# Kernel optimization log

Hardware: AMD Instinct MI355X
Metric: run time of the kernel (lower is better)

The kernel has to match this reference:

```python
import jax, jax.numpy as jnp
import numpy as np

N_HEAD = 16
ROPE_BASE = 10000.0


def _rope(x):
    # x: (B, T, H, D), interleaved even/odd (GPT-NeoX style)
    B, T, H, D = x.shape
    inv_freq = 1.0 / (ROPE_BASE ** (jnp.arange(0, D, 2, dtype=jnp.float32) / D))
    t = jnp.arange(T, dtype=jnp.float32)
    freqs = t[:, None] * inv_freq[None, :]            # (T, D//2)
    cos = jnp.cos(freqs)[None, :, None, :]            # (1, T, 1, D//2)
    sin = jnp.sin(freqs)[None, :, None, :]
    x1, x2 = x[..., ::2], x[..., 1::2]
    y1 = x1 * cos - x2 * sin
    y2 = x1 * sin + x2 * cos
    return jnp.stack((y1, y2), axis=-1).reshape(B, T, H, D)


def setup_inputs() -> dict:
    key = jax.random.key(0)
    k1, k2, k3 = jax.random.split(key, 3)
    B, T, C = 4, 2048, 1024
    x = jax.random.normal(k1, (B, T, C), dtype=jnp.float32)
    W_attn = jax.random.normal(k2, (C, 3 * C), dtype=jnp.float32) * (1.0 / np.sqrt(C))
    W_proj = jax.random.normal(k3, (C, C), dtype=jnp.float32) * (1.0 / np.sqrt(C))
    return {"x": x, "W_attn": W_attn, "W_proj": W_proj}


def reference(x, W_attn, W_proj):
    B, T, C = x.shape
    H = N_HEAD
    D = C // H
    qkv = jnp.einsum('btc,cf->btf', x, W_attn)        # (B, T, 3C)
    q, k, v = jnp.split(qkv, 3, axis=-1)
    q = _rope(q.reshape(B, T, H, D))
    k = _rope(k.reshape(B, T, H, D))
    v = v.reshape(B, T, H, D)
    # (B, H, T, D)
    q = q.transpose(0, 2, 1, 3)
    k = k.transpose(0, 2, 1, 3)
    v = v.transpose(0, 2, 1, 3)
    scale = 1.0 / np.sqrt(D).astype(np.float32)
    scores = jnp.einsum('bhqd,bhkd->bhqk', q, k) * scale
    causal = jnp.tril(jnp.ones((T, T), dtype=bool))
    scores = jnp.where(causal[None, None], scores, jnp.finfo(scores.dtype).min)
    att = jax.nn.softmax(scores, axis=-1)
    y = jnp.einsum('bhqk,bhkd->bhqd', att, v)         # (B, H, T, D)
    y = y.transpose(0, 2, 1, 3).reshape(B, T, C)
    return jnp.einsum('btc,cf->btf', y, W_proj)
```

## Files before the change

### kernel.cpp

```cpp
#include <hip/hip_runtime.h>
#include <hip/hip_bf16.h>
#include <math.h>

typedef __attribute__((ext_vector_type(8))) __bf16 bf16x8;
typedef __attribute__((ext_vector_type(4))) float f32x4;
typedef __attribute__((ext_vector_type(16))) float f32x16;
typedef __attribute__((ext_vector_type(4))) unsigned short us4;

#define DEVINL static __device__ __forceinline__

DEVINL unsigned short f2bf(float f) {
  union { float f; unsigned int u; } v; v.f = f;
  return (unsigned short)((v.u + 0x7FFFu + ((v.u >> 16) & 1u)) >> 16);
}

DEVINL unsigned short f2bf_hw(float f) {
  __bf16 h = (__bf16)f;
  union { __bf16 h; unsigned short u; } v; v.h = h;
  return v.u;
}

DEVINL unsigned pk2(float a, float b) {
  return (unsigned)f2bf_hw(a) | ((unsigned)f2bf_hw(b) << 16);
}

DEVINL f32x4 mfma16(bf16x8 a, bf16x8 b, f32x4 c) {
  return __builtin_amdgcn_mfma_f32_16x16x32_bf16(a, b, c, 0, 0, 0);
}
DEVINL f32x16 mfma32(bf16x8 a, bf16x8 b, f32x16 c) {
  return __builtin_amdgcn_mfma_f32_32x32x16_bf16(a, b, c, 0, 0, 0);
}

#define GLOAD16(GP, LP)                                                        \
  __builtin_amdgcn_global_load_lds(                                            \
      (const __attribute__((address_space(1))) void*)(GP),                     \
      (__attribute__((address_space(3))) void*)(LP), 16, 0, 0)

static constexpr int kB = 4, kT = 2048, kC = 1024, kH = 16, kD = 64;
static constexpr int kM = kB * kT;

__global__ void cvt_x_kernel(const float* __restrict__ x,
                             unsigned short* __restrict__ xb, int n4) {
  int stride = gridDim.x * blockDim.x;
  for (int i = blockIdx.x * blockDim.x + threadIdx.x; i < n4; i += stride) {
    float4 v = ((const float4*)x)[i];
    us4 o;
    o[0] = f2bf(v.x); o[1] = f2bf(v.y); o[2] = f2bf(v.z); o[3] = f2bf(v.w);
    ((us4*)xb)[i] = o;
  }
}

__global__ void transpose_w_kernel(const float* __restrict__ W,
                                   unsigned short* __restrict__ WT,
                                   int K, int N) {
  __shared__ float tile[32][33];
  int n0 = blockIdx.x * 32, k0 = blockIdx.y * 32;
  int tx = threadIdx.x, ty = threadIdx.y;
#pragma unroll
  for (int i = 0; i < 4; ++i)
    tile[ty + i * 8][tx] = W[(size_t)(k0 + ty + i * 8) * N + n0 + tx];
  __syncthreads();
#pragma unroll
  for (int i = 0; i < 4; ++i)
    WT[(size_t)(n0 + ty + i * 8) * K + k0 + tx] = f2bf(tile[tx][ty + i * 8]);
}

__global__ void rope_table_kernel(float* __restrict__ cosT,
                                  float* __restrict__ sinT) {
  int idx = blockIdx.x * blockDim.x + threadIdx.x;
  if (idx >= kT * 32) return;
  int d2 = idx >> 11, t = idx & 2047;
  double ang = (double)t * pow(10000.0, -(double)d2 / 32.0);
  cosT[idx] = (float)cos(ang);
  sinT[idx] = (float)sin(ang);
}

template <int EPI>
__global__ __launch_bounds__(256) void gemm_bt_kernel(
    const unsigned short* __restrict__ A, const unsigned short* __restrict__ Bt,
    float* __restrict__ Cout, int Ndim, int Kdim,
    const float* __restrict__ cosT, const float* __restrict__ sinT,
    unsigned short* __restrict__ Qr, unsigned short* __restrict__ Kr,
    unsigned short* __restrict__ Vtg) {
  __shared__ unsigned short As[3][128 * 32];
  __shared__ unsigned short Bs[3][128 * 32];
  const int tid = threadIdx.x;
  const int wave = tid >> 6, lane = tid & 63;

  const int nwg = gridDim.x * gridDim.y;
  const int lin = blockIdx.y * gridDim.x + blockIdx.x;
  const int wg = (lin & 7) * (nwg >> 3) + (lin >> 3);
  const int n0 = (wg % gridDim.x) * 128, m0 = (wg / gridDim.x) * 128;

  const int wr = wave >> 1, wc = wave & 1;

  f32x4 acc[4][4] = {};

  const int srow = lane >> 2;
  const int kcol = (lane & 3) * 8;
  const int fr = lane & 15, kk8 = (lane >> 4) * 8;

  auto stage = [&](int k0, int bb) {
#pragma unroll
    for (int o = 0; o < 2; ++o) {
      int s = o * 4 + wave;
      int row = s * 16 + srow;
      GLOAD16(A + (size_t)(m0 + row) * Kdim + k0 + kcol, &As[bb][s * 512]);
      GLOAD16(Bt + (size_t)(n0 + row) * Kdim + k0 + kcol, &Bs[bb][s * 512]);
    }
  };

  const int NT = Kdim >> 5;
  stage(0, 0);
  stage(32, 1);

  for (int t = 0; t < NT; ++t) {
    const int buf = t % 3;
    if (t + 1 < NT) {
      asm volatile("s_waitcnt vmcnt(4)" ::: "memory");
    } else {
      asm volatile("s_waitcnt vmcnt(0)" ::: "memory");
    }
    __builtin_amdgcn_sched_barrier(0);
    __builtin_amdgcn_s_barrier();
    if (t + 2 < NT) stage((t + 2) << 5, (t + 2) % 3);

    bf16x8 af[4], bfr[4];
#pragma unroll
    for (int f = 0; f < 4; ++f)
      af[f] = *(const bf16x8*)&As[buf][(wr * 64 + f * 16 + fr) * 32 + kk8];
#pragma unroll
    for (int f = 0; f < 4; ++f)
      bfr[f] = *(const bf16x8*)&Bs[buf][(wc * 64 + f * 16 + fr) * 32 + kk8];
#pragma unroll
    for (int i = 0; i < 4; ++i)
#pragma unroll
      for (int j = 0; j < 4; ++j)
        acc[i][j] = mfma16(af[i], bfr[j], acc[i][j]);

    asm volatile("s_waitcnt lgkmcnt(0)" ::: "memory");
    __builtin_amdgcn_sched_barrier(0);
  }

  const int lr = (lane >> 4) * 4;
  const int fc = lane & 15;
  if (EPI == 0) {
#pragma unroll
    for (int i = 0; i < 4; ++i) {
      int mb = m0 + wr * 64 + i * 16 + lr;
#pragma unroll
      for (int j = 0; j < 4; ++j) {
        int n = n0 + wc * 64 + j * 16 + fc;
#pragma unroll
        for (int r = 0; r < 4; ++r)
          Cout[(size_t)(mb + r) * Ndim + n] = acc[i][j][r];
      }
    }
  } else {
#pragma unroll
    for (int i = 0; i < 4; ++i) {
      int mb = m0 + wr * 64 + i * 16 + lr;
      int b = mb >> 11, t0 = mb & 2047;
#pragma unroll
      for (int j = 0; j < 4; ++j) {
        int n = n0 + wc * 64 + j * 16 + fc;
        int sec = n >> 10;
        int c = n & 1023;
        int h = c >> 6, d = c & 63;
        size_t bh = (size_t)(b * 16 + h);
        if (sec == 2) {
          us4 pk;
#pragma unroll
          for (int r = 0; r < 4; ++r) pk[r] = f2bf(acc[i][j][r]);
          *(us4*)&Vtg[(bh * 64 + d) * 2048 + t0] = pk;
        } else {
          unsigned short* dst = (sec == 0) ? Qr : Kr;
          float4 c4 = *(const float4*)&cosT[(d >> 1) * 2048 + t0];
          float4 s4 = *(const float4*)&sinT[(d >> 1) * 2048 + t0];
          const float* cp = (const float*)&c4;
          const float* sp = (const float*)&s4;
#pragma unroll
          for (int r = 0; r < 4; ++r) {
            float v = acc[i][j][r];
            float pv = __shfl_xor(v, 1);
            float y = (d & 1) ? fmaf(pv, sp[r], v * cp[r])
                              : fmaf(v, cp[r], -pv * sp[r]);
            dst[(bh * 2048 + t0 + r) * 64 + d] = f2bf(y);
          }
        }
      }
    }
  }
}

__global__ __launch_bounds__(256, 2)
void attn_kernel(const unsigned short* __restrict__ Qr,
                 const unsigned short* __restrict__ Kr,
                 const unsigned short* __restrict__ Vtg,
                 unsigned short* __restrict__ Yb) {
  __shared__ unsigned short Ks[2][64 * 64];
  __shared__ unsigned short Vs[2][64 * 64];

  const int tid = threadIdx.x;
  const int wave = tid >> 6, lane = tid & 63;
  const int q31 = lane & 31, hi = lane >> 5;
  const int srow = lane >> 3;
  const int sblk = (lane & 7) ^ srow;
  const int rswz = (lane & 7) << 4;

  int lin = blockIdx.y * 8 + blockIdx.x;
  int wg = (lin & 7) * 64 + (lin >> 3);
  const int qpair = wg & 7;
  const int bh = wg >> 3;

  const unsigned short* Qg = Qr + (size_t)bh * 2048 * 64;
  const unsigned short* Kg = Kr + (size_t)bh * 2048 * 64;
  const unsigned short* Vg = Vtg + (size_t)bh * 64 * 2048;

  const float c = 0.18033688f;
  const float THR = 44.0f;

  auto stage = [&](int j, int bb) {
    int kv0s = j * 64;
#pragma unroll
    for (int o = 0; o < 2; ++o) {
      int s = o * 4 + wave;
      int row = s * 8 + srow;
      GLOAD16(Kg + ((size_t)(kv0s + row) * 64 + sblk * 8), &Ks[bb][s * 512]);
      GLOAD16(Vg + ((size_t)row * 2048 + kv0s + sblk * 8), &Vs[bb][s * 512]);
    }
  };

  for (int seg = 0; seg < 2; ++seg) {
    const int qblk = seg ? (15 - qpair) : qpair;
    const int q0 = qblk * 128;
    const int qw = q0 + wave * 32;
    const int qg = qw + q31;
    const int NT = 2 * qblk + 2;

    bf16x8 qf[4];
#pragma unroll
    for (int ds = 0; ds < 4; ++ds)
      qf[ds] = *(const bf16x8*)&Qg[(size_t)qg * 64 + ds * 16 + hi * 8];

    float mrow = -1e30f, lrow = 0.f;
    f32x16 y0 = {}, y1 = {};

    stage(0, 0);
    asm volatile("s_waitcnt vmcnt(0)" ::: "memory");
    __syncthreads();

    for (int t = 0; t < NT; ++t) {
      const int buf = t & 1;
      if (t + 1 < NT) stage(t + 1, buf ^ 1);
      const int kv0 = t * 64;

      if (kv0 <= qw + 31) {
        f32x16 st[2] = {};
        __builtin_amdgcn_s_setprio(1);
#pragma unroll
        for (int sub = 0; sub < 2; ++sub) {
          const unsigned char* kbase =
              (const unsigned char*)Ks[buf] + (sub * 32 + q31) * 128;
#pragma unroll
          for (int ds = 0; ds < 4; ++ds) {
            bf16x8 af = *(const bf16x8*)(kbase + ((ds * 32 + hi * 16) ^ rswz));
            st[sub] = mfma32(af, qf[ds], st[sub]);
          }
        }
        __builtin_amdgcn_s_setprio(0);

        if (kv0 + 63 > qw) {
#pragma unroll
          for (int sub = 0; sub < 2; ++sub)
#pragma unroll
            for (int r = 0; r < 16; ++r) {
              int kv = kv0 + sub * 32 + (r & 3) + 8 * (r >> 2) + 4 * hi;
              if (kv > qg) st[sub][r] = -1e30f;
            }
        }

        float tm = st[0][0];
#pragma unroll
        for (int r = 1; r < 16; ++r) tm = fmaxf(tm, st[0][r]);
#pragma unroll
        for (int r = 0; r < 16; ++r) tm = fmaxf(tm, st[1][r]);
        tm = fmaxf(tm, __shfl_xor(tm, 32));

        if (!__all(tm <= mrow + THR)) {
          float mn = fmaxf(mrow, tm);
          float al = __builtin_amdgcn_exp2f((mrow - mn) * c);
          mrow = mn;
          lrow *= al;
#pragma unroll
          for (int r = 0; r < 16; ++r) { y0[r] *= al; y1[r] *= al; }
        }

        const float mc = mrow * c;
        float ps = 0.f;
        unsigned pkw[2][8];
#pragma unroll
        for (int sub = 0; sub < 2; ++sub)
#pragma unroll
          for (int j = 0; j < 8; ++j) {
            float pa = __builtin_amdgcn_exp2f(fmaf(st[sub][2 * j], c, -mc));
            float pb = __builtin_amdgcn_exp2f(fmaf(st[sub][2 * j + 1], c, -mc));
            ps += pa + pb;
            pkw[sub][j] = pk2(pa, pb);
          }
        ps += __shfl_xor(ps, 32);
        lrow += ps;

        __builtin_amdgcn_s_setprio(1);
#pragma unroll
        for (int sub = 0; sub < 2; ++sub) {
#pragma unroll
          for (int ksl = 0; ksl < 2; ++ksl) {
            unsigned w0 = pkw[sub][ksl * 4 + 0], w2 = pkw[sub][ksl * 4 + 2];
            unsigned w1 = pkw[sub][ksl * 4 + 1], w3 = pkw[sub][ksl * 4 + 3];
            asm volatile("v_permlane32_swap_b32 %0, %1" : "+v"(w0), "+v"(w2));
            asm volatile("v_permlane32_swap_b32 %0, %1" : "+v"(w1), "+v"(w3));
            union { bf16x8 v; unsigned u[4]; } pf;
            pf.u[0] = w0; pf.u[1] = w1; pf.u[2] = w2; pf.u[3] = w3;
            const int cb = sub * 64 + ksl * 32 + hi * 16;
#pragma unroll
            for (int dm = 0; dm < 2; ++dm) {
              const int row = dm * 32 + q31;
              bf16x8 vf = *(const bf16x8*)((const unsigned char*)Vs[buf] +
                                           row * 128 + (cb ^ rswz));
              if (dm == 0) y0 = mfma32(vf, pf.v, y0);
              else         y1 = mfma32(vf, pf.v, y1);
            }
          }
        }
        __builtin_amdgcn_s_setprio(0);
      }

      __syncthreads();
    }

    const int b = bh >> 4, h = bh & 15;
    float inv = __builtin_amdgcn_rcpf(lrow);
    unsigned short* yrow = Yb + (size_t)(b * 2048 + qg) * 1024 + h * 64;
#pragma unroll
    for (int dm = 0; dm < 2; ++dm)
#pragma unroll
      for (int g = 0; g < 4; ++g) {
        us4 o;
#pragma unroll
        for (int e = 0; e < 4; ++e) {
          float yv = dm ? y1[g * 4 + e] : y0[g * 4 + e];
          o[e] = f2bf_hw(yv * inv);
        }
        *(us4*)&yrow[dm * 32 + g * 8 + hi * 4] = o;
      }
  }
}

extern "C" void kernel_launch(void* const* d_in, const int* in_sizes, int n_in,
                              void* d_out, int out_size, void* d_ws,
                              size_t ws_size, hipStream_t stream) {
  const float* x = (const float*)d_in[0];
  const float* Wa = (const float*)d_in[1];
  const float* Wp = (const float*)d_in[2];
  float* out = (float*)d_out;
  char* ws = (char*)d_ws;

  constexpr size_t OFF_WAT = 0;
  constexpr size_t OFF_WPT = 6291456;
  constexpr size_t OFF_COS = 8388608;
  constexpr size_t OFF_SIN = 8650752;
  constexpr size_t OFF_XB  = 8912896;
  constexpr size_t OFF_Q   = 25690112;
  constexpr size_t OFF_K   = 42467328;
  constexpr size_t OFF_V   = 59244544;

  unsigned short* WaT = (unsigned short*)(ws + OFF_WAT);
  unsigned short* WpT = (unsigned short*)(ws + OFF_WPT);
  float* cosT = (float*)(ws + OFF_COS);
  float* sinT = (float*)(ws + OFF_SIN);
  unsigned short* xb = (unsigned short*)(ws + OFF_XB);
  unsigned short* Yb = xb;
  unsigned short* Qr = (unsigned short*)(ws + OFF_Q);
  unsigned short* Kr = (unsigned short*)(ws + OFF_K);
  unsigned short* Vt = (unsigned short*)(ws + OFF_V);

  cvt_x_kernel<<<2048, 256, 0, stream>>>(x, xb, kM * kC / 4);
  transpose_w_kernel<<<dim3(96, 32), dim3(32, 8), 0, stream>>>(Wa, WaT, 1024, 3072);
  transpose_w_kernel<<<dim3(32, 32), dim3(32, 8), 0, stream>>>(Wp, WpT, 1024, 1024);
  rope_table_kernel<<<256, 256, 0, stream>>>(cosT, sinT);

  gemm_bt_kernel<1><<<dim3(24, 64), 256, 0, stream>>>(
      xb, WaT, nullptr, 3072, 1024, cosT, sinT, Qr, Kr, Vt);

  attn_kernel<<<dim3(8, 64), 256, 0, stream>>>(Qr, Kr, Vt, Yb);

  gemm_bt_kernel<0><<<dim3(8, 64), 256, 0, stream>>>(
      Yb, WpT, out, 1024, 1024, nullptr, nullptr, nullptr, nullptr, nullptr);
}
```

Before: 185.1 us.

## Use 256x256 GEMM tiles with 8 waves, 4-stage pipeline and LDS swizzle

Replaces the 128x128, 4-wave GEMM with a 256x256 tile run by 8 waves (512 threads), each wave computing 128x64 in two halves. Global loads use a 4-buffer ring issued three tiles ahead and are split across the two compute halves. LDS columns are XOR-swizzled to avoid bank conflicts, and s_setprio raises priority around the MFMA bursts. This raises data reuse per tile and overlaps loads with compute, but the larger LDS footprint (64KB) lowers occupancy and the grids become smaller (384 and 128 blocks), which can underfill the 256 CUs.

```diff
diff --git a/kernel.cpp b/kernel.cpp
--- a/kernel.cpp
+++ b/kernel.cpp
@@ -76,78 +76,107 @@
 }
 
 template <int EPI>
-__global__ __launch_bounds__(256) void gemm_bt_kernel(
+__global__ __launch_bounds__(512, 2) void gemm256_bt_kernel(
     const unsigned short* __restrict__ A, const unsigned short* __restrict__ Bt,
     float* __restrict__ Cout, int Ndim, int Kdim,
     const float* __restrict__ cosT, const float* __restrict__ sinT,
     unsigned short* __restrict__ Qr, unsigned short* __restrict__ Kr,
     unsigned short* __restrict__ Vtg) {
-  __shared__ unsigned short As[3][128 * 32];
-  __shared__ unsigned short Bs[3][128 * 32];
+  __shared__ unsigned short As[4][256 * 32];
+  __shared__ unsigned short Bs[4][256 * 32];
   const int tid = threadIdx.x;
   const int wave = tid >> 6, lane = tid & 63;
 
   const int nwg = gridDim.x * gridDim.y;
   const int lin = blockIdx.y * gridDim.x + blockIdx.x;
   const int wg = (lin & 7) * (nwg >> 3) + (lin >> 3);
-  const int n0 = (wg % gridDim.x) * 128, m0 = (wg / gridDim.x) * 128;
-
-  const int wr = wave >> 1, wc = wave & 1;
-
-  f32x4 acc[4][4] = {};
-
+  const int n0 = (wg % gridDim.x) * 256, m0 = (wg / gridDim.x) * 256;
+
+  const int wr = wave >> 2, wc = wave & 3;
+
+  f32x4 acc[8][4] = {};
+
+  const int fr = lane & 15;
+  const int kswz = (((lane >> 4) ^ ((lane >> 1) & 3)) << 3);
   const int srow = lane >> 2;
-  const int kcol = (lane & 3) * 8;
-  const int fr = lane & 15, kk8 = (lane >> 4) * 8;
-
-  auto stage = [&](int k0, int bb) {
-#pragma unroll
-    for (int o = 0; o < 2; ++o) {
-      int s = o * 4 + wave;
-      int row = s * 16 + srow;
-      GLOAD16(A + (size_t)(m0 + row) * Kdim + k0 + kcol, &As[bb][s * 512]);
-      GLOAD16(Bt + (size_t)(n0 + row) * Kdim + k0 + kcol, &Bs[bb][s * 512]);
-    }
+  const int scol = (((lane & 3) ^ ((lane >> 3) & 3)) << 3);
+
+  auto stage = [&](int t, int h) {
+    const int bb = t & 3;
+    const int k0 = t << 5;
+    const int s = h * 8 + wave;
+    const int row = s * 16 + srow;
+    GLOAD16(A + (size_t)(m0 + row) * Kdim + k0 + scol, &As[bb][s * 512]);
+    GLOAD16(Bt + (size_t)(n0 + row) * Kdim + k0 + scol, &Bs[bb][s * 512]);
   };
 
   const int NT = Kdim >> 5;
-  stage(0, 0);
-  stage(32, 1);
+
+  stage(0, 0); stage(0, 1);
+  stage(1, 0); stage(1, 1);
+  stage(2, 0); stage(2, 1);
+  asm volatile("s_waitcnt vmcnt(8)" ::: "memory");
+  __builtin_amdgcn_s_barrier();
 
   for (int t = 0; t < NT; ++t) {
-    const int buf = t % 3;
-    if (t + 1 < NT) {
-      asm volatile("s_waitcnt vmcnt(4)" ::: "memory");
-    } else {
-      asm volatile("s_waitcnt vmcnt(0)" ::: "memory");
-    }
+    const int bb = t & 3;
+    bf16x8 af[4], bfr[4];
+
+#pragma unroll
+    for (int j = 0; j < 4; ++j) {
+      int row = wc * 64 + j * 16 + fr;
+      bfr[j] = *(const bf16x8*)&Bs[bb][row * 32 + kswz];
+    }
+#pragma unroll
+    for (int i = 0; i < 4; ++i) {
+      int row = wr * 128 + i * 16 + fr;
+      af[i] = *(const bf16x8*)&As[bb][row * 32 + kswz];
+    }
+    if (t + 3 < NT) stage(t + 3, 0);
+    __builtin_amdgcn_s_barrier();
+    asm volatile("s_waitcnt lgkmcnt(0)" ::: "memory");
     __builtin_amdgcn_sched_barrier(0);
-    __builtin_amdgcn_s_barrier();
-    if (t + 2 < NT) stage((t + 2) << 5, (t + 2) % 3);
-
-    bf16x8 af[4], bfr[4];
-#pragma unroll
-    for (int f = 0; f < 4; ++f)
-      af[f] = *(const bf16x8*)&As[buf][(wr * 64 + f * 16 + fr) * 32 + kk8];
-#pragma unroll
-    for (int f = 0; f < 4; ++f)
-      bfr[f] = *(const bf16x8*)&Bs[buf][(wc * 64 + f * 16 + fr) * 32 + kk8];
+    __builtin_amdgcn_s_setprio(1);
 #pragma unroll
     for (int i = 0; i < 4; ++i)
 #pragma unroll
       for (int j = 0; j < 4; ++j)
         acc[i][j] = mfma16(af[i], bfr[j], acc[i][j]);
-
+    __builtin_amdgcn_s_setprio(0);
+    __builtin_amdgcn_s_barrier();
+
+#pragma unroll
+    for (int i = 0; i < 4; ++i) {
+      int row = wr * 128 + (4 + i) * 16 + fr;
+      af[i] = *(const bf16x8*)&As[bb][row * 32 + kswz];
+    }
+    if (t + 3 < NT) stage(t + 3, 1);
+    __builtin_amdgcn_s_barrier();
     asm volatile("s_waitcnt lgkmcnt(0)" ::: "memory");
     __builtin_amdgcn_sched_barrier(0);
+    __builtin_amdgcn_s_setprio(1);
+#pragma unroll
+    for (int i = 0; i < 4; ++i)
+#pragma unroll
+      for (int j = 0; j < 4; ++j)
+        acc[4 + i][j] = mfma16(af[i], bfr[j], acc[4 + i][j]);
+    __builtin_amdgcn_s_setprio(0);
+    if (t + 3 < NT) {
+      asm volatile("s_waitcnt vmcnt(8)" ::: "memory");
+    } else if (t + 2 < NT) {
+      asm volatile("s_waitcnt vmcnt(4)" ::: "memory");
+    } else if (t + 1 < NT) {
+      asm volatile("s_waitcnt vmcnt(0)" ::: "memory");
+    }
+    __builtin_amdgcn_s_barrier();
   }
 
   const int lr = (lane >> 4) * 4;
   const int fc = lane & 15;
   if (EPI == 0) {
 #pragma unroll
-    for (int i = 0; i < 4; ++i) {
-      int mb = m0 + wr * 64 + i * 16 + lr;
+    for (int i = 0; i < 8; ++i) {
+      int mb = m0 + wr * 128 + i * 16 + lr;
 #pragma unroll
       for (int j = 0; j < 4; ++j) {
         int n = n0 + wc * 64 + j * 16 + fc;
@@ -158,8 +187,8 @@
     }
   } else {
 #pragma unroll
-    for (int i = 0; i < 4; ++i) {
-      int mb = m0 + wr * 64 + i * 16 + lr;
+    for (int i = 0; i < 8; ++i) {
+      int mb = m0 + wr * 128 + i * 16 + lr;
       int b = mb >> 11, t0 = mb & 2047;
 #pragma unroll
       for (int j = 0; j < 4; ++j) {
@@ -390,11 +419,11 @@
   transpose_w_kernel<<<dim3(32, 32), dim3(32, 8), 0, stream>>>(Wp, WpT, 1024, 1024);
   rope_table_kernel<<<256, 256, 0, stream>>>(cosT, sinT);
 
-  gemm_bt_kernel<1><<<dim3(24, 64), 256, 0, stream>>>(
+  gemm256_bt_kernel<1><<<dim3(12, 32), 512, 0, stream>>>(
       xb, WaT, nullptr, 3072, 1024, cosT, sinT, Qr, Kr, Vt);
 
   attn_kernel<<<dim3(8, 64), 256, 0, stream>>>(Qr, Kr, Vt, Yb);
 
-  gemm_bt_kernel<0><<<dim3(8, 64), 256, 0, stream>>>(
+  gemm256_bt_kernel<0><<<dim3(4, 32), 512, 0, stream>>>(
       Yb, WpT, out, 1024, 1024, nullptr, nullptr, nullptr, nullptr, nullptr);
 }
```

After: 201.3 us. +8.7%, slower.
